# Kernel tuning notes

Hardware: AMD Instinct MI355X
Metric: run time of the kernel (lower is better)

Reference implementation:

```python
import jax, jax.numpy as jnp
import numpy as np

D_MODEL = 1024
N_HEADS = 16
D_HEAD = D_MODEL // N_HEADS


def setup_inputs() -> dict:
    key = jax.random.key(0)
    k_x, k_wqkv, k_bqkv, k_wo, k_bo = jax.random.split(key, 5)
    B, T = 2, 2048
    scale = 1.0 / np.sqrt(D_MODEL)
    return {
        "x": jax.random.normal(k_x, (B, T, D_MODEL), dtype=jnp.float32),
        "w_qkv": jax.random.uniform(k_wqkv, (D_MODEL, 3 * D_MODEL), jnp.float32, -scale, scale),
        "b_qkv": jax.random.uniform(k_bqkv, (3 * D_MODEL,), jnp.float32, -scale, scale),
        "w_out": jax.random.uniform(k_wo, (D_MODEL, D_MODEL), jnp.float32, -scale, scale),
        "b_out": jax.random.uniform(k_bo, (D_MODEL,), jnp.float32, -scale, scale),
    }


def reference(x, w_qkv, b_qkv, w_out, b_out):
    B, T, D = x.shape
    qkv = x @ w_qkv + b_qkv                      # [B,T,3D]
    q, k, v = jnp.split(qkv, 3, axis=-1)
    # [B,T,D] -> [B,H,T,d]
    def split_heads(t):
        return t.reshape(B, T, N_HEADS, D_HEAD).transpose(0, 2, 1, 3)
    q, k, v = split_heads(q), split_heads(k), split_heads(v)
    scores = jnp.einsum('bhqd,bhkd->bhqk', q, k) / np.sqrt(D_HEAD)
    probs = jax.nn.softmax(scores, axis=-1)      # dropout p=0 (eval)
    out = jnp.einsum('bhqk,bhkd->bhqd', probs, v)
    out = out.transpose(0, 2, 1, 3).reshape(B, T, D)
    return out @ w_out + b_out
```

## Files before the change

### kernel.cpp

```cpp
#include <hip/hip_runtime.h>
#include <hip/hip_bf16.h>
#include <math.h>

#define D_MODEL 1024
#define N_HEADS 16
#define D_HEAD  64
#define SEQ     2048
#define NBATCH  2
#define NROWS   (NBATCH * SEQ)

#define C2F 0.18033688011112042f

typedef __attribute__((ext_vector_type(8))) short short8v;
typedef __attribute__((ext_vector_type(4))) float f32x4;
typedef __attribute__((ext_vector_type(16))) float f32x16;
typedef __attribute__((ext_vector_type(4))) unsigned int u32x4;

__device__ __forceinline__ unsigned short f2bf(float x) {
    unsigned int u = __float_as_uint(x);
    return (unsigned short)((u + 0x7FFFu + ((u >> 16) & 1u)) >> 16);
}
__device__ __forceinline__ void split_bf(float x, unsigned short& hi, unsigned short& lo) {
    unsigned int u = __float_as_uint(x);
    unsigned int ht = u & 0xFFFF0000u;
    hi = (unsigned short)(ht >> 16);
    lo = f2bf(x - __uint_as_float(ht));
}
__device__ __forceinline__ unsigned int cvtpk(float lo, float hi) {
    unsigned int r;
    asm("v_cvt_pk_bf16_f32 %0, %1, %2" : "=v"(r) : "v"(lo), "v"(hi));
    return r;
}
__device__ __forceinline__ short8v u2s(u32x4 v) {
    union { u32x4 u; short8v s; } c; c.u = v; return c.s;
}

__global__ __launch_bounds__(256) void splitT_kernel(
    const float* __restrict__ W, unsigned short* __restrict__ Th,
    unsigned short* __restrict__ Tl, int K, int N, int qcols, int write_lo)
{
    __shared__ float tile[64][68];
    const int tid = threadIdx.x;
    const int nbn = N >> 6;
    const int k0 = (blockIdx.x / nbn) << 6;
    const int n0 = (blockIdx.x % nbn) << 6;
    const int r  = tid >> 4;
    const int c4 = (tid & 15) * 4;

#pragma unroll
    for (int i = 0; i < 4; ++i) {
        float4 v = *(const float4*)(W + (size_t)(k0 + r + i * 16) * N + n0 + c4);
        *(float4*)&tile[r + i * 16][c4] = v;
    }
    __syncthreads();

    const int kl = (tid & 15) * 4;
#pragma unroll
    for (int i = 0; i < 4; ++i) {
        const int nl = (tid >> 4) + i * 16;
        const float sc = (n0 + nl < qcols) ? C2F : 1.0f;
        if (write_lo) {
            ushort4 h4, l4;
            unsigned short h, l;
            split_bf(tile[kl + 0][nl] * sc, h, l); h4.x = h; l4.x = l;
            split_bf(tile[kl + 1][nl] * sc, h, l); h4.y = h; l4.y = l;
            split_bf(tile[kl + 2][nl] * sc, h, l); h4.z = h; l4.z = l;
            split_bf(tile[kl + 3][nl] * sc, h, l); h4.w = h; l4.w = l;
            *(ushort4*)(Th + (size_t)(n0 + nl) * K + k0 + kl) = h4;
            *(ushort4*)(Tl + (size_t)(n0 + nl) * K + k0 + kl) = l4;
        } else {
            ushort4 h4;
            h4.x = f2bf(tile[kl + 0][nl] * sc);
            h4.y = f2bf(tile[kl + 1][nl] * sc);
            h4.z = f2bf(tile[kl + 2][nl] * sc);
            h4.w = f2bf(tile[kl + 3][nl] * sc);
            *(ushort4*)(Th + (size_t)(n0 + nl) * K + k0 + kl) = h4;
        }
    }
}

#define ASTRIDE 40

__global__ __launch_bounds__(256) void gemm_xw_kernel(
    const float* __restrict__ A,
    const unsigned short* __restrict__ Bth,
    const float* __restrict__ bias,
    unsigned short* __restrict__ C, int M, int N, int K, int qcols)
{
    __shared__ __align__(16) unsigned short Ab[128][ASTRIDE];
    __shared__ __align__(16) unsigned short Bh[128][ASTRIDE];

    const int tid  = threadIdx.x;
    const int wave = tid >> 6;
    const int lane = tid & 63;
    const int col  = lane & 15;
    const int q4   = lane >> 4;
    const int wm   = (wave >> 1) * 64;
    const int wn   = (wave & 1) * 64;

    const int nwg = gridDim.x;
    const int cpx = nwg >> 3;
    const int swz = (blockIdx.x & 7) * cpx + (blockIdx.x >> 3);
    const int nbn = N / 128;
    const int bm = (swz / nbn) * 128;
    const int bn = (swz % nbn) * 128;

    const int sr = tid >> 1;
    const int sq = (tid & 1) * 16;
    const float* aptr = A + (size_t)(bm + sr) * K + sq;
    const unsigned short* bhp = Bth + (size_t)(bn + sr) * K + sq;

    f32x4 acc[4][4];
#pragma unroll
    for (int i = 0; i < 4; ++i)
#pragma unroll
        for (int j = 0; j < 4; ++j) acc[i][j] = (f32x4){0.f, 0.f, 0.f, 0.f};

    float4 a0, a1, a2, a3;
    short8v b0h, b1h;

#define G1LOAD(k0) { \
    a0 = *(const float4*)(aptr + (k0)); \
    a1 = *(const float4*)(aptr + (k0) + 4); \
    a2 = *(const float4*)(aptr + (k0) + 8); \
    a3 = *(const float4*)(aptr + (k0) + 12); \
    b0h = *(const short8v*)(bhp + (k0)); \
    b1h = *(const short8v*)(bhp + (k0) + 8); \
}

#define G1WRITE() { \
    u32x4 p0, p1; \
    p0.x = cvtpk(a0.x, a0.y); p0.y = cvtpk(a0.z, a0.w); \
    p0.z = cvtpk(a1.x, a1.y); p0.w = cvtpk(a1.z, a1.w); \
    p1.x = cvtpk(a2.x, a2.y); p1.y = cvtpk(a2.z, a2.w); \
    p1.z = cvtpk(a3.x, a3.y); p1.w = cvtpk(a3.z, a3.w); \
    *(u32x4*)&Ab[sr][sq]     = p0; \
    *(u32x4*)&Ab[sr][sq + 8] = p1; \
    *(short8v*)&Bh[sr][sq]     = b0h; \
    *(short8v*)&Bh[sr][sq + 8] = b1h; \
}

#define G1COMP() { \
    short8v af[4]; \
    _Pragma("unroll") \
    for (int mt = 0; mt < 4; ++mt) \
        af[mt] = *(const short8v*)&Ab[wm + mt * 16 + col][q4 * 8]; \
    _Pragma("unroll") \
    for (int nt = 0; nt < 4; ++nt) { \
        short8v bhf = *(const short8v*)&Bh[wn + nt * 16 + col][q4 * 8]; \
        _Pragma("unroll") \
        for (int mt = 0; mt < 4; ++mt) \
            acc[mt][nt] = __builtin_amdgcn_mfma_f32_16x16x32_bf16(af[mt], bhf, acc[mt][nt], 0, 0, 0); \
    } \
}

    G1LOAD(0);
    G1WRITE();
    for (int k0 = 32; k0 < K; k0 += 32) {
        G1LOAD(k0);
        __syncthreads();
        G1COMP();
        __syncthreads();
        G1WRITE();
    }
    __syncthreads();
    G1COMP();
#undef G1LOAD
#undef G1WRITE
#undef G1COMP

    const float bscale = (bn < qcols) ? C2F : 1.0f;
    float bv[4];
#pragma unroll
    for (int nt = 0; nt < 4; ++nt) bv[nt] = bias[bn + wn + nt * 16 + col] * bscale;

#pragma unroll
    for (int mt = 0; mt < 4; ++mt)
#pragma unroll
        for (int r = 0; r < 4; ++r) {
            const int row = bm + wm + mt * 16 + q4 * 4 + r;
#pragma unroll
            for (int nt = 0; nt < 4; ++nt)
                C[(size_t)row * N + bn + wn + nt * 16 + col] = f2bf(acc[mt][nt][r] + bv[nt]);
        }
}

__global__ __launch_bounds__(256) void gemm_ao_kernel(
    const unsigned short* __restrict__ Aoh,
    const unsigned short* __restrict__ Aol,
    const unsigned short* __restrict__ Bth,
    const unsigned short* __restrict__ Btl,
    const float* __restrict__ bias,
    float* __restrict__ C, int M, int N, int K)
{
    __shared__ __align__(16) unsigned short Ah[128][ASTRIDE];
    __shared__ __align__(16) unsigned short Al[128][ASTRIDE];
    __shared__ __align__(16) unsigned short Bh[128][ASTRIDE];
    __shared__ __align__(16) unsigned short Bl[128][ASTRIDE];

    const int tid  = threadIdx.x;
    const int wave = tid >> 6;
    const int lane = tid & 63;
    const int col  = lane & 15;
    const int q4   = lane >> 4;
    const int wm   = (wave >> 1) * 64;
    const int wn   = (wave & 1) * 64;

    const int nwg = gridDim.x;
    const int cpx = nwg >> 3;
    const int swz = (blockIdx.x & 7) * cpx + (blockIdx.x >> 3);
    const int nbn = N / 128;
    const int bm = (swz / nbn) * 128;
    const int bn = (swz % nbn) * 128;

    const int sr = tid >> 1;
    const int sq = (tid & 1) * 16;
    const unsigned short* ahp = Aoh + (size_t)(bm + sr) * K + sq;
    const unsigned short* alp = Aol + (size_t)(bm + sr) * K + sq;
    const unsigned short* bhp = Bth + (size_t)(bn + sr) * K + sq;
    const unsigned short* blp = Btl + (size_t)(bn + sr) * K + sq;

    f32x4 acc[4][4];
#pragma unroll
    for (int i = 0; i < 4; ++i)
#pragma unroll
        for (int j = 0; j < 4; ++j) acc[i][j] = (f32x4){0.f, 0.f, 0.f, 0.f};

    short8v a0h, a1h, a0l, a1l, b0h, b1h, b0l, b1l;

#define G2LOAD(k0) { \
    a0h = *(const short8v*)(ahp + (k0)); \
    a1h = *(const short8v*)(ahp + (k0) + 8); \
    a0l = *(const short8v*)(alp + (k0)); \
    a1l = *(const short8v*)(alp + (k0) + 8); \
    b0h = *(const short8v*)(bhp + (k0)); \
    b1h = *(const short8v*)(bhp + (k0) + 8); \
    b0l = *(const short8v*)(blp + (k0)); \
    b1l = *(const short8v*)(blp + (k0) + 8); \
}

#define G2WRITE() { \
    *(short8v*)&Ah[sr][sq]     = a0h; \
    *(short8v*)&Ah[sr][sq + 8] = a1h; \
    *(short8v*)&Al[sr][sq]     = a0l; \
    *(short8v*)&Al[sr][sq + 8] = a1l; \
    *(short8v*)&Bh[sr][sq]     = b0h; \
    *(short8v*)&Bh[sr][sq + 8] = b1h; \
    *(short8v*)&Bl[sr][sq]     = b0l; \
    *(short8v*)&Bl[sr][sq + 8] = b1l; \
}

#define G2COMP() { \
    short8v ahf[4], alf[4]; \
    _Pragma("unroll") \
    for (int mt = 0; mt < 4; ++mt) { \
        ahf[mt] = *(const short8v*)&Ah[wm + mt * 16 + col][q4 * 8]; \
        alf[mt] = *(const short8v*)&Al[wm + mt * 16 + col][q4 * 8]; \
    } \
    _Pragma("unroll") \
    for (int nt = 0; nt < 4; ++nt) { \
        short8v bhf = *(const short8v*)&Bh[wn + nt * 16 + col][q4 * 8]; \
        short8v blf = *(const short8v*)&Bl[wn + nt * 16 + col][q4 * 8]; \
        _Pragma("unroll") \
        for (int mt = 0; mt < 4; ++mt) { \
            acc[mt][nt] = __builtin_amdgcn_mfma_f32_16x16x32_bf16(ahf[mt], bhf, acc[mt][nt], 0, 0, 0); \
            acc[mt][nt] = __builtin_amdgcn_mfma_f32_16x16x32_bf16(alf[mt], bhf, acc[mt][nt], 0, 0, 0); \
            acc[mt][nt] = __builtin_amdgcn_mfma_f32_16x16x32_bf16(ahf[mt], blf, acc[mt][nt], 0, 0, 0); \
        } \
    } \
}

    G2LOAD(0);
    G2WRITE();
    for (int k0 = 32; k0 < K; k0 += 32) {
        G2LOAD(k0);
        __syncthreads();
        G2COMP();
        __syncthreads();
        G2WRITE();
    }
    __syncthreads();
    G2COMP();
#undef G2LOAD
#undef G2WRITE
#undef G2COMP

    float bv[4];
#pragma unroll
    for (int nt = 0; nt < 4; ++nt) bv[nt] = bias[bn + wn + nt * 16 + col];

#pragma unroll
    for (int mt = 0; mt < 4; ++mt)
#pragma unroll
        for (int r = 0; r < 4; ++r) {
            const int row = bm + wm + mt * 16 + q4 * 4 + r;
#pragma unroll
            for (int nt = 0; nt < 4; ++nt)
                C[(size_t)row * N + bn + wn + nt * 16 + col] = acc[mt][nt][r] + bv[nt];
        }
}

__global__ __launch_bounds__(128) void attn_mfma_kernel(
    const unsigned short* __restrict__ qkv,
    unsigned short* __restrict__ aoh, unsigned short* __restrict__ aol)
{
    __shared__ __align__(16) unsigned short Ks[64 * 64];
    __shared__ __align__(16) unsigned short Vt[64 * 64];

    const int tid  = threadIdx.x;
    const int wave = tid >> 6;
    const int lane = tid & 63;
    const int l31  = lane & 31;
    const int lh   = lane >> 5;
    const bool hihalf = (lh != 0);

    const int bh = blockIdx.x;
    const int qt = blockIdx.y;
    const int b = bh >> 4;
    const int h = bh & 15;
    const int qrow0 = b * SEQ + qt * 64 + wave * 32;
    const int krow0 = b * SEQ;

    short8v qf[4];
    {
        const unsigned short* qsrc = qkv + (size_t)(qrow0 + l31) * (3 * D_MODEL) + h * 64 + lh * 8;
#pragma unroll
        for (int s = 0; s < 4; ++s)
            qf[s] = *(const short8v*)(qsrc + s * 16);
    }

    const int krow  = tid >> 1;
    const int khalf = (tid & 1) * 32;
    const int vk0   = (tid & 15) * 4;
    const int vd0   = (tid >> 4) * 8;

    f32x16 ot0, ot1;
#pragma unroll
    for (int r = 0; r < 16; ++r) { ot0[r] = 0.f; ot1[r] = 0.f; }
    float ll = 0.f;

    short8v kg[4], vg[4];
    const int swr = (lane & 7) << 3;

#define ALOAD(c) { \
    const unsigned short* ksrc = qkv + (size_t)(krow0 + (c) * 64 + krow) * (3 * D_MODEL) \
                                 + D_MODEL + h * 64 + khalf; \
    kg[0] = ((const short8v*)ksrc)[0]; \
    kg[1] = ((const short8v*)ksrc)[1]; \
    kg[2] = ((const short8v*)ksrc)[2]; \
    kg[3] = ((const short8v*)ksrc)[3]; \
    _Pragma("unroll") \
    for (int i2 = 0; i2 < 4; ++i2) \
        vg[i2] = *(const short8v*)(qkv + (size_t)(krow0 + (c) * 64 + vk0 + i2) * (3 * D_MODEL) \
                                   + 2 * D_MODEL + h * 64 + vd0); \
}

#define AWRITE() { \
    const int base = krow * 64 + khalf; \
    const int sw = (krow & 7) << 3; \
    *(short8v*)&Ks[(base)      ^ sw] = kg[0]; \
    *(short8v*)&Ks[(base + 8)  ^ sw] = kg[1]; \
    *(short8v*)&Ks[(base + 16) ^ sw] = kg[2]; \
    *(short8v*)&Ks[(base + 24) ^ sw] = kg[3]; \
    _Pragma("unroll") \
    for (int j = 0; j < 8; ++j) { \
        ushort4 w; \
        w.x = ((const unsigned short*)&vg[0])[j]; \
        w.y = ((const unsigned short*)&vg[1])[j]; \
        w.z = ((const unsigned short*)&vg[2])[j]; \
        w.w = ((const unsigned short*)&vg[3])[j]; \
        const int d = vd0 + j; \
        *(ushort4*)&Vt[(d * 64 + vk0) ^ ((d & 7) << 3)] = w; \
    } \
}

#define ACOMPUTE() { \
    f32x16 st0, st1; \
    _Pragma("unroll") for (int r = 0; r < 16; ++r) { st0[r] = 0.f; st1[r] = 0.f; } \
    _Pragma("unroll") \
    for (int s = 0; s < 4; ++s) { \
        short8v kf0 = *(const short8v*)&Ks[(l31 * 64 + s * 16 + lh * 8) ^ swr]; \
        st0 = __builtin_amdgcn_mfma_f32_32x32x16_bf16(kf0, qf[s], st0, 0, 0, 0); \
    } \
    _Pragma("unroll") \
    for (int s = 0; s < 4; ++s) { \
        short8v kf1 = *(const short8v*)&Ks[((32 + l31) * 64 + s * 16 + lh * 8) ^ swr]; \
        st1 = __builtin_amdgcn_mfma_f32_32x32x16_bf16(kf1, qf[s], st1, 0, 0, 0); \
    } \
    float rs = 0.f; \
    _Pragma("unroll") \
    for (int r = 0; r < 16; ++r) { \
        st0[r] = __builtin_exp2f(st0[r]); \
        rs += st0[r]; \
    } \
    _Pragma("unroll") \
    for (int r = 0; r < 16; ++r) { \
        st1[r] = __builtin_exp2f(st1[r]); \
        rs += st1[r]; \
    } \
    rs += __shfl_xor(rs, 32); \
    ll += rs; \
    unsigned int pk0[8], pk1[8], x0[8], x1[8]; \
    _Pragma("unroll") \
    for (int i2 = 0; i2 < 8; ++i2) { \
        pk0[i2] = cvtpk(st0[2 * i2], st0[2 * i2 + 1]); \
        pk1[i2] = cvtpk(st1[2 * i2], st1[2 * i2 + 1]); \
    } \
    _Pragma("unroll") \
    for (int i2 = 0; i2 < 8; ++i2) { \
        x0[i2] = (unsigned int)__shfl_xor((int)pk0[i2], 32); \
        x1[i2] = (unsigned int)__shfl_xor((int)pk1[i2], 32); \
    } \
    u32x4 pf[4]; \
    pf[0].x = hihalf ? x0[2] : pk0[0];  pf[0].y = hihalf ? x0[3] : pk0[1]; \
    pf[0].z = hihalf ? pk0[2] : x0[0];  pf[0].w = hihalf ? pk0[3] : x0[1]; \
    pf[1].x = hihalf ? x0[6] : pk0[4];  pf[1].y = hihalf ? x0[7] : pk0[5]; \
    pf[1].z = hihalf ? pk0[6] : x0[4];  pf[1].w = hihalf ? pk0[7] : x0[5]; \
    pf[2].x = hihalf ? x1[2] : pk1[0];  pf[2].y = hihalf ? x1[3] : pk1[1]; \
    pf[2].z = hihalf ? pk1[2] : x1[0];  pf[2].w = hihalf ? pk1[3] : x1[1]; \
    pf[3].x = hihalf ? x1[6] : pk1[4];  pf[3].y = hihalf ? x1[7] : pk1[5]; \
    pf[3].z = hihalf ? pk1[6] : x1[4];  pf[3].w = hihalf ? pk1[7] : x1[5]; \
    _Pragma("unroll") \
    for (int ks2 = 0; ks2 < 4; ++ks2) { \
        const short8v pfr = u2s(pf[ks2]); \
        const int keyoff = ks2 * 16 + lh * 8; \
        short8v vf0 = *(const short8v*)&Vt[(l31 * 64 + keyoff) ^ swr]; \
        ot0 = __builtin_amdgcn_mfma_f32_32x32x16_bf16(vf0, pfr, ot0, 0, 0, 0); \
        short8v vf1 = *(const short8v*)&Vt[((32 + l31) * 64 + keyoff) ^ swr]; \
        ot1 = __builtin_amdgcn_mfma_f32_32x32x16_bf16(vf1, pfr, ot1, 0, 0, 0); \
    } \
}

    ALOAD(0);
    AWRITE();
    for (int i = 0; i < 31; ++i) {
        ALOAD(i + 1);
        __syncthreads();
        ACOMPUTE();
        __syncthreads();
        AWRITE();
    }
    __syncthreads();
    ACOMPUTE();
#undef ALOAD
#undef AWRITE
#undef ACOMPUTE

    const float il = 1.0f / ll;
    const int qrow = qrow0 + l31;
    unsigned short* dh = aoh + (size_t)qrow * D_MODEL + h * 64;
    unsigned short* dl = aol + (size_t)qrow * D_MODEL + h * 64;
#pragma unroll
    for (int r = 0; r < 16; ++r) {
        const int dloc = (r & 3) + 8 * (r >> 2) + 4 * lh;
        unsigned short hh, lo2;
        split_bf(ot0[r] * il, hh, lo2);
        dh[dloc] = hh; dl[dloc] = lo2;
        split_bf(ot1[r] * il, hh, lo2);
        dh[32 + dloc] = hh; dl[32 + dloc] = lo2;
    }
}

extern "C" void kernel_launch(void* const* d_in, const int* in_sizes, int n_in,
                              void* d_out, int out_size, void* d_ws, size_t ws_size,
                              hipStream_t stream) {
    (void)in_sizes; (void)n_in; (void)out_size; (void)ws_size;

    const float* x     = (const float*)d_in[0];
    const float* w_qkv = (const float*)d_in[1];
    const float* b_qkv = (const float*)d_in[2];
    const float* w_out = (const float*)d_in[3];
    const float* b_out = (const float*)d_in[4];
    float* out = (float*)d_out;

    char* ws = (char*)d_ws;
    unsigned short* qkv_bf  = (unsigned short*)(ws);
    unsigned short* aoh     = (unsigned short*)(ws + 25165824);
    unsigned short* aol     = (unsigned short*)(ws + 33554432);
    unsigned short* wqkvT_h = (unsigned short*)(ws + 41943040);
    unsigned short* woutT_h = (unsigned short*)(ws + 48234496);
    unsigned short* woutT_l = (unsigned short*)(ws + 50331648);

    splitT_kernel<<<dim3((D_MODEL / 64) * (3 * D_MODEL / 64)), 256, 0, stream>>>(
        w_qkv, wqkvT_h, (unsigned short*)nullptr, D_MODEL, 3 * D_MODEL, D_MODEL, 0);
    splitT_kernel<<<dim3((D_MODEL / 64) * (D_MODEL / 64)), 256, 0, stream>>>(
        w_out, woutT_h, woutT_l, D_MODEL, D_MODEL, 0, 1);

    gemm_xw_kernel<<<dim3((NROWS / 128) * (3 * D_MODEL / 128)), 256, 0, stream>>>(
        x, wqkvT_h, b_qkv, qkv_bf, NROWS, 3 * D_MODEL, D_MODEL, D_MODEL);

    attn_mfma_kernel<<<dim3(NBATCH * N_HEADS, SEQ / 64), 128, 0, stream>>>(qkv_bf, aoh, aol);

    gemm_ao_kernel<<<dim3((NROWS / 128) * (D_MODEL / 128)), 256, 0, stream>>>(
        aoh, aol, woutT_h, woutT_l, b_out, out, NROWS, D_MODEL, D_MODEL);
}
```

Baseline: 165.9 us.

## Double-buffer K/V shared tiles and prefetch two chunks ahead in attention

The attention kernel now keeps two LDS buffers for K and V^T and two register staging sets, so each iteration computes on one buffer while writing the other and issuing global loads two chunks ahead. This cuts the barriers per chunk from two to one and gives global loads more time to land before use. In exchange it doubles LDS use, raises register pressure from the extra staging arrays, and issues redundant clamped loads near the end of the loop.

```diff
diff --git a/kernel.cpp b/kernel.cpp
--- a/kernel.cpp
+++ b/kernel.cpp
@@ -304,8 +304,8 @@
     const unsigned short* __restrict__ qkv,
     unsigned short* __restrict__ aoh, unsigned short* __restrict__ aol)
 {
-    __shared__ __align__(16) unsigned short Ks[64 * 64];
-    __shared__ __align__(16) unsigned short Vt[64 * 64];
+    __shared__ __align__(16) unsigned short Ks[2][64 * 64];
+    __shared__ __align__(16) unsigned short Vt[2][64 * 64];
 
     const int tid  = threadIdx.x;
     const int wave = tid >> 6;
@@ -339,11 +339,12 @@
     for (int r = 0; r < 16; ++r) { ot0[r] = 0.f; ot1[r] = 0.f; }
     float ll = 0.f;
 
-    short8v kg[4], vg[4];
+    short8v kgA[4], vgA[4], kgB[4], vgB[4];
     const int swr = (lane & 7) << 3;
 
-#define ALOAD(c) { \
-    const unsigned short* ksrc = qkv + (size_t)(krow0 + (c) * 64 + krow) * (3 * D_MODEL) \
+#define ALOAD(kg, vg, c) { \
+    const int cc = ((c) < 32) ? (c) : 31; \
+    const unsigned short* ksrc = qkv + (size_t)(krow0 + cc * 64 + krow) * (3 * D_MODEL) \
                                  + D_MODEL + h * 64 + khalf; \
     kg[0] = ((const short8v*)ksrc)[0]; \
     kg[1] = ((const short8v*)ksrc)[1]; \
@@ -351,17 +352,17 @@
     kg[3] = ((const short8v*)ksrc)[3]; \
     _Pragma("unroll") \
     for (int i2 = 0; i2 < 4; ++i2) \
-        vg[i2] = *(const short8v*)(qkv + (size_t)(krow0 + (c) * 64 + vk0 + i2) * (3 * D_MODEL) \
+        vg[i2] = *(const short8v*)(qkv + (size_t)(krow0 + cc * 64 + vk0 + i2) * (3 * D_MODEL) \
                                    + 2 * D_MODEL + h * 64 + vd0); \
 }
 
-#define AWRITE() { \
+#define AWRITE(buf, kg, vg) { \
     const int base = krow * 64 + khalf; \
     const int sw = (krow & 7) << 3; \
-    *(short8v*)&Ks[(base)      ^ sw] = kg[0]; \
-    *(short8v*)&Ks[(base + 8)  ^ sw] = kg[1]; \
-    *(short8v*)&Ks[(base + 16) ^ sw] = kg[2]; \
-    *(short8v*)&Ks[(base + 24) ^ sw] = kg[3]; \
+    *(short8v*)&Ks[buf][(base)      ^ sw] = kg[0]; \
+    *(short8v*)&Ks[buf][(base + 8)  ^ sw] = kg[1]; \
+    *(short8v*)&Ks[buf][(base + 16) ^ sw] = kg[2]; \
+    *(short8v*)&Ks[buf][(base + 24) ^ sw] = kg[3]; \
     _Pragma("unroll") \
     for (int j = 0; j < 8; ++j) { \
         ushort4 w; \
@@ -370,21 +371,21 @@
         w.z = ((const unsigned short*)&vg[2])[j]; \
         w.w = ((const unsigned short*)&vg[3])[j]; \
         const int d = vd0 + j; \
-        *(ushort4*)&Vt[(d * 64 + vk0) ^ ((d & 7) << 3)] = w; \
-    } \
-}
-
-#define ACOMPUTE() { \
+        *(ushort4*)&Vt[buf][(d * 64 + vk0) ^ ((d & 7) << 3)] = w; \
+    } \
+}
+
+#define ACOMPUTE(buf) { \
     f32x16 st0, st1; \
     _Pragma("unroll") for (int r = 0; r < 16; ++r) { st0[r] = 0.f; st1[r] = 0.f; } \
     _Pragma("unroll") \
     for (int s = 0; s < 4; ++s) { \
-        short8v kf0 = *(const short8v*)&Ks[(l31 * 64 + s * 16 + lh * 8) ^ swr]; \
+        short8v kf0 = *(const short8v*)&Ks[buf][(l31 * 64 + s * 16 + lh * 8) ^ swr]; \
         st0 = __builtin_amdgcn_mfma_f32_32x32x16_bf16(kf0, qf[s], st0, 0, 0, 0); \
     } \
     _Pragma("unroll") \
     for (int s = 0; s < 4; ++s) { \
-        short8v kf1 = *(const short8v*)&Ks[((32 + l31) * 64 + s * 16 + lh * 8) ^ swr]; \
+        short8v kf1 = *(const short8v*)&Ks[buf][((32 + l31) * 64 + s * 16 + lh * 8) ^ swr]; \
         st1 = __builtin_amdgcn_mfma_f32_32x32x16_bf16(kf1, qf[s], st1, 0, 0, 0); \
     } \
     float rs = 0.f; \
@@ -424,24 +425,30 @@
     for (int ks2 = 0; ks2 < 4; ++ks2) { \
         const short8v pfr = u2s(pf[ks2]); \
         const int keyoff = ks2 * 16 + lh * 8; \
-        short8v vf0 = *(const short8v*)&Vt[(l31 * 64 + keyoff) ^ swr]; \
+        short8v vf0 = *(const short8v*)&Vt[buf][(l31 * 64 + keyoff) ^ swr]; \
         ot0 = __builtin_amdgcn_mfma_f32_32x32x16_bf16(vf0, pfr, ot0, 0, 0, 0); \
-        short8v vf1 = *(const short8v*)&Vt[((32 + l31) * 64 + keyoff) ^ swr]; \
+        short8v vf1 = *(const short8v*)&Vt[buf][((32 + l31) * 64 + keyoff) ^ swr]; \
         ot1 = __builtin_amdgcn_mfma_f32_32x32x16_bf16(vf1, pfr, ot1, 0, 0, 0); \
     } \
 }
 
-    ALOAD(0);
-    AWRITE();
-    for (int i = 0; i < 31; ++i) {
-        ALOAD(i + 1);
+    ALOAD(kgA, vgA, 0);
+    AWRITE(0, kgA, vgA);
+    ALOAD(kgA, vgA, 1);
+    ALOAD(kgB, vgB, 2);
+    __syncthreads();
+
+    for (int i = 0; i < 32; i += 2) {
+        ACOMPUTE(0);
+        AWRITE(1, kgA, vgA);
+        ALOAD(kgA, vgA, i + 3);
         __syncthreads();
-        ACOMPUTE();
+
+        ACOMPUTE(1);
+        AWRITE(0, kgB, vgB);
+        ALOAD(kgB, vgB, i + 4);
         __syncthreads();
-        AWRITE();
-    }
-    __syncthreads();
-    ACOMPUTE();
+    }
 #undef ALOAD
 #undef AWRITE
 #undef ACOMPUTE
```

New measurement: 167.3 us. Within noise of the previous version (+0.9%).
